# Performance work log

Hardware: AMD Instinct MI355X
Metric: run time of the kernel (lower is better)

Reference implementation:

```python
import jax, jax.numpy as jnp
import numpy as np

N_NODES = 50000
N_EDGES = 800000
D = 128          # input_dim == output_dim
H = 2 * D        # hidden size = 2*output_dim
EPS = 1e-5       # BatchNorm1d eps


def _mlp(x, W1, b1, g1, beta1, W2, b2):
    # Linear -> BatchNorm1d (training-mode batch stats) -> ReLU -> Linear
    y = x @ W1 + b1
    mu = jnp.mean(y, axis=0)
    var = jnp.mean(jnp.square(y - mu), axis=0)  # biased var, as used for normalization
    y = (y - mu) * jax.lax.rsqrt(var + EPS) * g1 + beta1
    y = jax.nn.relu(y)
    return y @ W2 + b2


def setup_inputs() -> dict:
    key = jax.random.key(0)
    ks = jax.random.split(key, 16)
    h = jax.random.normal(ks[0], (N_NODES, D), dtype=jnp.float32)
    e = jax.random.normal(ks[1], (N_EDGES, D), dtype=jnp.float32)
    src = jax.random.randint(ks[2], (N_EDGES,), 0, N_NODES, dtype=jnp.int32)
    dst = jax.random.randint(ks[3], (N_EDGES,), 0, N_NODES, dtype=jnp.int32)

    def lin(k, fan_in, fan_out):
        return jax.random.normal(k, (fan_in, fan_out), dtype=jnp.float32) * (1.0 / np.sqrt(fan_in))

    params = {
        # mlp_bond: in 2D -> H -> D
        'W1b': lin(ks[4], 2 * D, H), 'b1b': jnp.zeros((H,), jnp.float32),
        'g1b': jnp.ones((H,), jnp.float32), 'beta1b': jnp.zeros((H,), jnp.float32),
        'W2b': lin(ks[5], H, D), 'b2b': jnp.zeros((D,), jnp.float32),
        # mlp_atom: in 2D -> H -> D
        'W1a': lin(ks[6], 2 * D, H), 'b1a': jnp.zeros((H,), jnp.float32),
        'g1a': jnp.ones((H,), jnp.float32), 'beta1a': jnp.zeros((H,), jnp.float32),
        'W2a': lin(ks[7], H, D), 'b2a': jnp.zeros((D,), jnp.float32),
    }
    return {'h': h, 'e': e, 'src': src, 'dst': dst, **params}


def reference(h, e, src, dst,
              W1b, b1b, g1b, beta1b, W2b, b2b,
              W1a, b1a, g1a, beta1a, W2a, b2a):
    # --- bond update: gather u_add_v, concat with e, MLP ---
    sum_h_edge = h[src] + h[dst]                              # [E, D]
    e_new = _mlp(jnp.concatenate([sum_h_edge, e], axis=-1),
                 W1b, b1b, g1b, beta1b, W2b, b2b)             # [E, D]

    # --- atom update: scatter-sum of src node feats and NEW edge feats to dst ---
    sum_h = jax.ops.segment_sum(h[src], dst, num_segments=N_NODES)   # copy_u + sum
    sum_e = jax.ops.segment_sum(e_new, dst, num_segments=N_NODES)   # copy_e + sum
    h_new = _mlp(jnp.concatenate([sum_h, sum_e], axis=-1),
                 W1a, b1a, g1a, beta1a, W2a, b2a)             # [N, D]

    # out_batch_norm=False, out_activation=None, residual=False, dropout=None
    return h_new, e_new
```

## Files before the change

kernel.cpp:

```cpp
#include <hip/hip_runtime.h>
#include <hip/hip_bf16.h>
#include <stdint.h>

#define DD 128
#define HH 256
#define EPSBN 1e-5f

typedef __attribute__((ext_vector_type(4))) float f32x4;
typedef __attribute__((ext_vector_type(8))) short s16x8;
typedef __attribute__((ext_vector_type(4))) short s16x4;

__device__ __forceinline__ unsigned short f2bf(float f){
  union { __hip_bfloat16 h; unsigned short u; } v;
  v.h = __float2bfloat16(f);
  return v.u;
}
__device__ __forceinline__ float bf2f(unsigned short s){
  union{unsigned u; float f;} v; v.u=((unsigned)s)<<16; return v.f;
}
__device__ __forceinline__ int swz(int row, int kb){ return row*512 + (kb ^ ((row&31)<<4)); }

__global__ void wt_kernel(const float* __restrict__ W1b, const float* __restrict__ W2b,
                          const float* __restrict__ W1a, const float* __restrict__ W2a,
                          unsigned short* __restrict__ WT1b, unsigned short* __restrict__ WT2b,
                          unsigned short* __restrict__ WT1a, unsigned short* __restrict__ WT2a){
  int idx = blockIdx.x*256 + threadIdx.x;
  if (idx < 65536){ int n=idx>>8, k=idx&255; WT1b[n*256+k]=f2bf(W1b[k*256+n]); }
  else if (idx < 98304){ int t=idx-65536; int n=t>>8, k=t&255; WT2b[n*256+k]=f2bf(W2b[k*128+n]); }
  else if (idx < 163840){ int t=idx-98304; int n=t>>8, k=t&255; WT1a[n*256+k]=f2bf(W1a[k*256+n]); }
  else if (idx < 196608){ int t=idx-163840; int n=t>>8, k=t&255; WT2a[n*256+k]=f2bf(W2a[k*128+n]); }
}

__global__ void h2bf_kernel(const float* __restrict__ h, unsigned short* __restrict__ hb, int n8){
  int i = blockIdx.x*256 + threadIdx.x;
  if (i < n8){
    f32x4 a = *(const f32x4*)(h + (size_t)i*8);
    f32x4 b = *(const f32x4*)(h + (size_t)i*8 + 4);
    s16x8 p;
    #pragma unroll
    for (int q=0;q<4;q++){ p[q]=(short)f2bf(a[q]); p[4+q]=(short)f2bf(b[q]); }
    *(s16x8*)(hb + (size_t)i*8) = p;
  }
}

__global__ void hist_kernel(const int* __restrict__ dst, int* __restrict__ counts, int E){
  int i = blockIdx.x*256 + threadIdx.x;
  if (i < E) atomicAdd(&counts[dst[i]], 1);
}

__global__ void scan_kernel(const int* __restrict__ counts, int* __restrict__ offsets,
                            int* __restrict__ cursor, int n){
  __shared__ int wsum[16];
  int tid = threadIdx.x, lane = tid&63, wid = tid>>6;
  int carry = 0;
  int nch = (n + 1023)/1024;
  for (int ch=0; ch<nch; ch++){
    int i = ch*1024 + tid;
    int v = (i<n)? counts[i] : 0;
    int s = v;
    #pragma unroll
    for (int off=1; off<64; off<<=1){ int t = __shfl_up(s, off); if (lane>=off) s += t; }
    if (lane==63) wsum[wid] = s;
    __syncthreads();
    int woff = 0, tot = 0;
    #pragma unroll
    for (int w=0; w<16; w++){ int t = wsum[w]; if (w<wid) woff += t; tot += t; }
    if (i<n){ int excl = carry + woff + s - v; offsets[i]=excl; cursor[i]=excl; }
    carry += tot;
    __syncthreads();
  }
  if (tid==0) offsets[n] = carry;
}

__global__ void fill_kernel(const int* __restrict__ dst, int* __restrict__ cursor,
                            int* __restrict__ eids, int E){
  int i = blockIdx.x*256 + threadIdx.x;
  if (i < E){ int slot = atomicAdd(&cursor[dst[i]], 1); eids[slot] = i; }
}

__device__ __forceinline__ void gemm1_core(char* xt, const s16x8 (&Bf)[8][2],
                                           float bias0, float bias1,
                                           unsigned short* __restrict__ yout,
                                           float* __restrict__ stats,
                                           int base, int nrows)
{
  const int tid = threadIdx.x;
  const int l = tid&63, w = tid>>6, lr = l&15, lg = l>>4;
  const int nb = w*32;
  f32x4 acc[4][2];
  #pragma unroll
  for (int mt=0;mt<4;mt++)
    #pragma unroll
    for (int nt=0;nt<2;nt++) acc[mt][nt] = (f32x4){0.f,0.f,0.f,0.f};
  #pragma unroll
  for (int kc=0;kc<8;kc++){
    s16x8 af[4];
    #pragma unroll
    for (int mt=0;mt<4;mt++)
      af[mt] = *(const s16x8*)(xt + swz(mt*16 + lr, kc*64 + lg*16));
    #pragma unroll
    for (int nt=0;nt<2;nt++)
      #pragma unroll
      for (int mt=0;mt<4;mt++)
        acc[mt][nt] = __builtin_amdgcn_mfma_f32_16x16x32_bf16(af[mt], Bf[kc][nt], acc[mt][nt], 0,0,0);
  }
  float st1a=0.f, st1b=0.f, st2a=0.f, st2b=0.f;
  #pragma unroll
  for (int mt=0;mt<4;mt++)
    #pragma unroll
    for (int q=0;q<4;q++){
      float m = (base + mt*16 + lg*4 + q < nrows) ? 1.0f : 0.0f;
      float v0 = (acc[mt][0][q] + bias0)*m;
      float v1 = (acc[mt][1][q] + bias1)*m;
      st1a += v0; st2a += v0*v0;
      st1b += v1; st2b += v1*v1;
    }
  __syncthreads();
  #pragma unroll
  for (int mt=0;mt<4;mt++)
    #pragma unroll
    for (int q=0;q<4;q++){
      *(unsigned short*)(xt + (mt*16 + lg*4 + q)*512 + (nb + lr)*2)      = f2bf(acc[mt][0][q] + bias0);
      *(unsigned short*)(xt + (mt*16 + lg*4 + q)*512 + (nb + 16 + lr)*2) = f2bf(acc[mt][1][q] + bias1);
    }
  __syncthreads();
  #pragma unroll
  for (int it=0;it<4;it++){
    int off = it*8192 + tid*16;
    int row = off >> 9;
    if (base + row < nrows)
      *(s16x8*)((char*)yout + (size_t)base*512 + off) = *(const s16x8*)(xt + off);
  }
  {
    int rep = blockIdx.x & 63;
    float s;
    s = st1a; s += __shfl_xor(s,16); s += __shfl_xor(s,32);
    if (l < 16) atomicAdd(&stats[rep*512 + nb + lr], s);
    s = st2a; s += __shfl_xor(s,16); s += __shfl_xor(s,32);
    if (l < 16) atomicAdd(&stats[rep*512 + 256 + nb + lr], s);
    s = st1b; s += __shfl_xor(s,16); s += __shfl_xor(s,32);
    if (l < 16) atomicAdd(&stats[rep*512 + nb + 16 + lr], s);
    s = st2b; s += __shfl_xor(s,16); s += __shfl_xor(s,32);
    if (l < 16) atomicAdd(&stats[rep*512 + 256 + nb + 16 + lr], s);
  }
}

__global__ __launch_bounds__(512, 4) void edge_mlp1(
    const unsigned short* __restrict__ hb, const float* __restrict__ e,
    const int* __restrict__ src, const int* __restrict__ dstv,
    const unsigned short* __restrict__ WT1, const float* __restrict__ b1,
    unsigned short* __restrict__ yout, float* __restrict__ stats, int E)
{
  __shared__ alignas(16) char xt[32768];
  const int tid = threadIdx.x;
  const int l = tid&63, w = tid>>6, lr = l&15, lg = l>>4;
  const int nb = w*32;
  const int base = blockIdx.x*64;

  {
    const int cb = tid&31, r0 = tid>>5;
    #pragma unroll
    for (int k=0;k<4;k++){
      int r = r0 + k*16;
      f32x4 v = *(const f32x4*)(e + (size_t)(base+r)*DD + cb*4);
      s16x4 p;
      #pragma unroll
      for (int q=0;q<4;q++) p[q] = (short)f2bf(v[q]);
      *(s16x4*)(xt + swz(r, 256 + cb*8)) = p;
    }
  }
  {
    const int r = tid>>3, jj = tid&7;
    const int ei = base + r;
    int s_ = src[ei], d_ = dstv[ei];
    const s16x8* hs = (const s16x8*)(hb + (size_t)s_*DD) + jj*2;
    const s16x8* hd = (const s16x8*)(hb + (size_t)d_*DD) + jj*2;
    s16x8 a0=hs[0], a1=hs[1], c0=hd[0], c1=hd[1];
    s16x8 o0, o1;
    #pragma unroll
    for (int q=0;q<8;q++){
      o0[q] = (short)f2bf(bf2f((unsigned short)a0[q]) + bf2f((unsigned short)c0[q]));
      o1[q] = (short)f2bf(bf2f((unsigned short)a1[q]) + bf2f((unsigned short)c1[q]));
    }
    *(s16x8*)(xt + swz(r, jj*32))      = o0;
    *(s16x8*)(xt + swz(r, jj*32 + 16)) = o1;
  }
  s16x8 Bf[8][2];
  #pragma unroll
  for (int kc=0;kc<8;kc++)
    #pragma unroll
    for (int nt=0;nt<2;nt++)
      Bf[kc][nt] = *(const s16x8*)(WT1 + (size_t)(nb + nt*16 + lr)*256 + kc*32 + lg*8);
  float bias0 = b1[nb+lr], bias1 = b1[nb+16+lr];
  __syncthreads();
  gemm1_core(xt, Bf, bias0, bias1, yout, stats, base, E);
}

__global__ __launch_bounds__(512, 2) void node_mlp1(
    const unsigned short* __restrict__ hb, const float* __restrict__ enew,
    const int* __restrict__ src, const int* __restrict__ offsets, const int* __restrict__ eids,
    const unsigned short* __restrict__ WT1, const float* __restrict__ b1,
    unsigned short* __restrict__ yout, float* __restrict__ stats, int NN)
{
  __shared__ alignas(16) char xt[32768];
  const int tid = threadIdx.x;
  const int l = tid&63, w = tid>>6, lr = l&15, lg = l>>4;
  const int nb = w*32;
  const int base = blockIdx.x*64;
  const int r = tid>>3, jj = tid&7;
  const int node = base + r;

  float ah[16], ae[16];
  #pragma unroll
  for (int q=0;q<16;q++){ ah[q]=0.f; ae[q]=0.f; }
  if (node < NN){
    int beg = offsets[node], end = offsets[node+1];
    for (int p=beg;p<end;p++){
      int eid = eids[p];
      int s_ = src[eid];
      const s16x8* hs = (const s16x8*)(hb + (size_t)s_*DD + jj*16);
      const f32x4* ep = (const f32x4*)(enew + (size_t)eid*DD + jj*16);
      s16x8 a0 = hs[0], a1 = hs[1];
      f32x4 e0 = ep[0], e1 = ep[1], e2 = ep[2], e3 = ep[3];
      #pragma unroll
      for (int q=0;q<8;q++){ ah[q] += bf2f((unsigned short)a0[q]); ah[8+q] += bf2f((unsigned short)a1[q]); }
      #pragma unroll
      for (int q=0;q<4;q++){ ae[q] += e0[q]; ae[4+q] += e1[q]; ae[8+q] += e2[q]; ae[12+q] += e3[q]; }
    }
  }
  {
    s16x8 o0, o1;
    #pragma unroll
    for (int q=0;q<8;q++){ o0[q] = (short)f2bf(ah[q]); o1[q] = (short)f2bf(ah[8+q]); }
    *(s16x8*)(xt + swz(r, jj*32))      = o0;
    *(s16x8*)(xt + swz(r, jj*32 + 16)) = o1;
    #pragma unroll
    for (int q=0;q<8;q++){ o0[q] = (short)f2bf(ae[q]); o1[q] = (short)f2bf(ae[8+q]); }
    *(s16x8*)(xt + swz(r, 256 + jj*32))      = o0;
    *(s16x8*)(xt + swz(r, 256 + jj*32 + 16)) = o1;
  }
  s16x8 Bf[8][2];
  #pragma unroll
  for (int kc=0;kc<8;kc++)
    #pragma unroll
    for (int nt=0;nt<2;nt++)
      Bf[kc][nt] = *(const s16x8*)(WT1 + (size_t)(nb + nt*16 + lr)*256 + kc*32 + lg*8);
  float bias0 = b1[nb+lr], bias1 = b1[nb+16+lr];
  __syncthreads();
  gemm1_core(xt, Bf, bias0, bias1, yout, stats, base, NN);
}

__global__ void finalize_kernel(const float* __restrict__ stats, const float* __restrict__ g,
                                const float* __restrict__ beta, float* __restrict__ scale, float invcnt){
  __shared__ float red[512];
  int tid = threadIdx.x;
  float s = 0.f;
  for (int rep=0; rep<64; rep++) s += stats[rep*512 + tid];
  red[tid] = s;
  __syncthreads();
  if (tid < 256){
    float mu  = red[tid]*invcnt;
    float var = red[256+tid]*invcnt - mu*mu;
    float a = g[tid] * rsqrtf(var + EPSBN);
    float c = beta[tid] - mu*a;
    scale[2*tid] = a; scale[2*tid+1] = c;
  }
}

__global__ __launch_bounds__(512, 4) void mlp2_kernel(const unsigned short* y,
    const unsigned short* __restrict__ WT2, const float* __restrict__ b2,
    const float* __restrict__ scale, float* outp, int nrows)
{
  __shared__ alignas(16) char xt[32768];
  const int tid = threadIdx.x;
  const int l = tid&63, w = tid>>6, lr = l&15, lg = l>>4;
  const int nb = w*16;
  const int base0 = blockIdx.x*128;

  s16x8 Bf[8];
  #pragma unroll
  for (int kc=0;kc<8;kc++)
    Bf[kc] = *(const s16x8*)(WT2 + (size_t)(nb + lr)*HH + kc*32 + lg*8);
  float bias = b2[nb+lr];
  const int cb = tid&31, r0 = tid>>5;
  float sa[8], sc[8];
  #pragma unroll
  for (int q=0;q<8;q++){ sa[q]=scale[2*(cb*8+q)]; sc[q]=scale[2*(cb*8+q)+1]; }

  #pragma unroll 1
  for (int t=0;t<2;t++){
    const int base = base0 + t*64;
    #pragma unroll
    for (int k=0;k<4;k++){
      int r = r0 + k*16;
      s16x8 raw = {0,0,0,0,0,0,0,0};
      if (base + r < nrows) raw = *(const s16x8*)(y + (size_t)(base+r)*HH + cb*8);
      s16x8 o;
      #pragma unroll
      for (int q=0;q<8;q++){
        float f = fmaxf(bf2f((unsigned short)raw[q])*sa[q] + sc[q], 0.0f);
        o[q] = (short)f2bf(f);
      }
      *(s16x8*)(xt + swz(r, cb*16)) = o;
    }
    __syncthreads();
    f32x4 acc[4];
    #pragma unroll
    for (int mt=0;mt<4;mt++) acc[mt] = (f32x4){0.f,0.f,0.f,0.f};
    #pragma unroll
    for (int kc=0;kc<8;kc++){
      s16x8 af[4];
      #pragma unroll
      for (int mt=0;mt<4;mt++)
        af[mt] = *(const s16x8*)(xt + swz(mt*16 + lr, kc*64 + lg*16));
      #pragma unroll
      for (int mt=0;mt<4;mt++)
        acc[mt] = __builtin_amdgcn_mfma_f32_16x16x32_bf16(af[mt], Bf[kc], acc[mt], 0,0,0);
    }
    __syncthreads();
    #pragma unroll
    for (int mt=0;mt<4;mt++)
      #pragma unroll
      for (int q=0;q<4;q++)
        *(float*)(xt + (mt*16 + lg*4 + q)*512 + (nb + lr)*4) = acc[mt][q] + bias;
    __syncthreads();
    #pragma unroll
    for (int it=0;it<4;it++){
      int off = it*8192 + tid*16;
      int row = off >> 9;
      if (base + row < nrows)
        *(f32x4*)(outp + (size_t)(base+row)*DD + ((off&511)>>2)) = *(const f32x4*)(xt + off);
    }
    if (t==0) __syncthreads();
  }
}

extern "C" void kernel_launch(void* const* d_in, const int* in_sizes, int n_in,
                              void* d_out, int out_size, void* d_ws, size_t ws_size,
                              hipStream_t stream) {
  const float* h    = (const float*)d_in[0];
  const float* e    = (const float*)d_in[1];
  const int*   src  = (const int*)d_in[2];
  const int*   dst  = (const int*)d_in[3];
  const float* W1b  = (const float*)d_in[4];
  const float* b1b  = (const float*)d_in[5];
  const float* g1b  = (const float*)d_in[6];
  const float* beta1b=(const float*)d_in[7];
  const float* W2b  = (const float*)d_in[8];
  const float* b2b  = (const float*)d_in[9];
  const float* W1a  = (const float*)d_in[10];
  const float* b1a  = (const float*)d_in[11];
  const float* g1a  = (const float*)d_in[12];
  const float* beta1a=(const float*)d_in[13];
  const float* W2a  = (const float*)d_in[14];
  const float* b2a  = (const float*)d_in[15];

  const int E  = in_sizes[2];
  const int NN = in_sizes[0] / DD;

  char* ws = (char*)d_ws;
  unsigned short* WT1b = (unsigned short*)(ws + 0);
  unsigned short* WT2b = (unsigned short*)(ws + 131072);
  unsigned short* WT1a = (unsigned short*)(ws + 196608);
  unsigned short* WT2a = (unsigned short*)(ws + 327680);
  float* scaleE = (float*)(ws + 393216);
  float* scaleN = (float*)(ws + 395264);
  float* statsE = (float*)(ws + 397312);
  float* statsN = (float*)(ws + 528384);
  int* counts  = (int*)(ws + 659456);
  int* offsets = (int*)(ws + 860160);
  int* cursor  = (int*)(ws + 1060864);
  int* eids    = (int*)(ws + 1261568);
  unsigned short* ya = (unsigned short*)(ws + 4461568);
  unsigned short* hb = (unsigned short*)(ws + 30086144);

  float* outH = (float*)d_out;
  float* outE = outH + (size_t)NN * DD;
  unsigned short* yE = (unsigned short*)outE;

  hipMemsetAsync(ws + 397312, 0, 131072 + 131072 + 200704, stream);

  wt_kernel<<<768, 256, 0, stream>>>(W1b, W2b, W1a, W2a, WT1b, WT2b, WT1a, WT2a);
  h2bf_kernel<<<(NN*DD/8 + 255)/256, 256, 0, stream>>>(h, hb, NN*DD/8);
  hist_kernel<<<(E+255)/256, 256, 0, stream>>>(dst, counts, E);
  scan_kernel<<<1, 1024, 0, stream>>>(counts, offsets, cursor, NN);
  fill_kernel<<<(E+255)/256, 256, 0, stream>>>(dst, cursor, eids, E);

  const int tE64  = E/64;
  const int tE128 = E/128;
  const int tN64  = (NN + 63)/64;
  const int tN128 = (NN + 127)/128;

  edge_mlp1<<<tE64, 512, 0, stream>>>(hb, e, src, dst, WT1b, b1b, yE, statsE, E);
  finalize_kernel<<<1, 512, 0, stream>>>(statsE, g1b, beta1b, scaleE, 1.0f/(float)E);
  mlp2_kernel<<<tE128, 512, 0, stream>>>(yE, WT2b, b2b, scaleE, outE, E);
  node_mlp1<<<tN64, 512, 0, stream>>>(hb, outE, src, offsets, eids, WT1a, b1a, ya, statsN, NN);
  finalize_kernel<<<1, 512, 0, stream>>>(statsN, g1a, beta1a, scaleN, 1.0f/(float)NN);
  mlp2_kernel<<<tN128, 512, 0, stream>>>(ya, WT2a, b2a, scaleN, outH, NN);
}
```

Baseline: 799.0 us.

## Split node gather from node GEMM, pre-sort src ids, fuse histogram

```diff
diff --git a/kernel.cpp b/kernel.cpp
--- a/kernel.cpp
+++ b/kernel.cpp
@@ -31,7 +31,8 @@
   else if (idx < 196608){ int t=idx-163840; int n=t>>8, k=t&255; WT2a[n*256+k]=f2bf(W2a[k*128+n]); }
 }
 
-__global__ void h2bf_kernel(const float* __restrict__ h, unsigned short* __restrict__ hb, int n8){
+__global__ void h2bf_hist_kernel(const float* __restrict__ h, unsigned short* __restrict__ hb, int n8,
+                                 const int* __restrict__ dst, int* __restrict__ counts, int E){
   int i = blockIdx.x*256 + threadIdx.x;
   if (i < n8){
     f32x4 a = *(const f32x4*)(h + (size_t)i*8);
@@ -41,10 +42,6 @@
     for (int q=0;q<4;q++){ p[q]=(short)f2bf(a[q]); p[4+q]=(short)f2bf(b[q]); }
     *(s16x8*)(hb + (size_t)i*8) = p;
   }
-}
-
-__global__ void hist_kernel(const int* __restrict__ dst, int* __restrict__ counts, int E){
-  int i = blockIdx.x*256 + threadIdx.x;
   if (i < E) atomicAdd(&counts[dst[i]], 1);
 }
 
@@ -72,10 +69,15 @@
   if (tid==0) offsets[n] = carry;
 }
 
-__global__ void fill_kernel(const int* __restrict__ dst, int* __restrict__ cursor,
-                            int* __restrict__ eids, int E){
+__global__ void fill_kernel(const int* __restrict__ dst, const int* __restrict__ srcv,
+                            int* __restrict__ cursor,
+                            int* __restrict__ eids, int* __restrict__ esrc, int E){
   int i = blockIdx.x*256 + threadIdx.x;
-  if (i < E){ int slot = atomicAdd(&cursor[dst[i]], 1); eids[slot] = i; }
+  if (i < E){
+    int slot = atomicAdd(&cursor[dst[i]], 1);
+    eids[slot] = i;
+    esrc[slot] = srcv[i];
+  }
 }
 
 __device__ __forceinline__ void gemm1_core(char* xt, const s16x8 (&Bf)[8][2],
@@ -196,9 +198,50 @@
   gemm1_core(xt, Bf, bias0, bias1, yout, stats, base, E);
 }
 
-__global__ __launch_bounds__(512, 2) void node_mlp1(
+__global__ __launch_bounds__(256, 8) void node_gather(
     const unsigned short* __restrict__ hb, const float* __restrict__ enew,
-    const int* __restrict__ src, const int* __restrict__ offsets, const int* __restrict__ eids,
+    const int* __restrict__ offsets, const int* __restrict__ eids, const int* __restrict__ esrc,
+    unsigned short* __restrict__ xnode, int NN)
+{
+  const int tid = threadIdx.x;
+  const int r = tid>>3, jj = tid&7;
+  const int node = blockIdx.x*32 + r;
+  if (node >= NN) return;
+  float ah[16], ae[16];
+  #pragma unroll
+  for (int q=0;q<16;q++){ ah[q]=0.f; ae[q]=0.f; }
+  int beg = offsets[node], end = offsets[node+1];
+  if (beg < end){
+    int eid = eids[beg];
+    int s_  = esrc[beg];
+    for (int p = beg; p < end; p++){
+      int pn = (p+1 < end) ? p+1 : p;
+      int eid_n = eids[pn];
+      int s_n   = esrc[pn];
+      const s16x8* hs = (const s16x8*)(hb + (size_t)s_*DD + jj*16);
+      const f32x4* ep = (const f32x4*)(enew + (size_t)eid*DD + jj*16);
+      s16x8 a0 = hs[0], a1 = hs[1];
+      f32x4 e0 = ep[0], e1 = ep[1], e2 = ep[2], e3 = ep[3];
+      #pragma unroll
+      for (int q=0;q<8;q++){ ah[q] += bf2f((unsigned short)a0[q]); ah[8+q] += bf2f((unsigned short)a1[q]); }
+      #pragma unroll
+      for (int q=0;q<4;q++){ ae[q] += e0[q]; ae[4+q] += e1[q]; ae[8+q] += e2[q]; ae[12+q] += e3[q]; }
+      eid = eid_n; s_ = s_n;
+    }
+  }
+  s16x8 o0, o1;
+  #pragma unroll
+  for (int q=0;q<8;q++){ o0[q] = (short)f2bf(ah[q]); o1[q] = (short)f2bf(ah[8+q]); }
+  *(s16x8*)(xnode + (size_t)node*HH + jj*16)     = o0;
+  *(s16x8*)(xnode + (size_t)node*HH + jj*16 + 8) = o1;
+  #pragma unroll
+  for (int q=0;q<8;q++){ o0[q] = (short)f2bf(ae[q]); o1[q] = (short)f2bf(ae[8+q]); }
+  *(s16x8*)(xnode + (size_t)node*HH + 128 + jj*16)     = o0;
+  *(s16x8*)(xnode + (size_t)node*HH + 128 + jj*16 + 8) = o1;
+}
+
+__global__ __launch_bounds__(512, 4) void node_gemm1(
+    const unsigned short* __restrict__ xnode,
     const unsigned short* __restrict__ WT1, const float* __restrict__ b1,
     unsigned short* __restrict__ yout, float* __restrict__ stats, int NN)
 {
@@ -207,37 +250,14 @@
   const int l = tid&63, w = tid>>6, lr = l&15, lg = l>>4;
   const int nb = w*32;
   const int base = blockIdx.x*64;
-  const int r = tid>>3, jj = tid&7;
-  const int node = base + r;
-
-  float ah[16], ae[16];
-  #pragma unroll
-  for (int q=0;q<16;q++){ ah[q]=0.f; ae[q]=0.f; }
-  if (node < NN){
-    int beg = offsets[node], end = offsets[node+1];
-    for (int p=beg;p<end;p++){
-      int eid = eids[p];
-      int s_ = src[eid];
-      const s16x8* hs = (const s16x8*)(hb + (size_t)s_*DD + jj*16);
-      const f32x4* ep = (const f32x4*)(enew + (size_t)eid*DD + jj*16);
-      s16x8 a0 = hs[0], a1 = hs[1];
-      f32x4 e0 = ep[0], e1 = ep[1], e2 = ep[2], e3 = ep[3];
-      #pragma unroll
-      for (int q=0;q<8;q++){ ah[q] += bf2f((unsigned short)a0[q]); ah[8+q] += bf2f((unsigned short)a1[q]); }
-      #pragma unroll
-      for (int q=0;q<4;q++){ ae[q] += e0[q]; ae[4+q] += e1[q]; ae[8+q] += e2[q]; ae[12+q] += e3[q]; }
-    }
-  }
-  {
-    s16x8 o0, o1;
-    #pragma unroll
-    for (int q=0;q<8;q++){ o0[q] = (short)f2bf(ah[q]); o1[q] = (short)f2bf(ah[8+q]); }
-    *(s16x8*)(xt + swz(r, jj*32))      = o0;
-    *(s16x8*)(xt + swz(r, jj*32 + 16)) = o1;
-    #pragma unroll
-    for (int q=0;q<8;q++){ o0[q] = (short)f2bf(ae[q]); o1[q] = (short)f2bf(ae[8+q]); }
-    *(s16x8*)(xt + swz(r, 256 + jj*32))      = o0;
-    *(s16x8*)(xt + swz(r, 256 + jj*32 + 16)) = o1;
+
+  #pragma unroll
+  for (int it=0;it<4;it++){
+    int off = it*8192 + tid*16;
+    int row = off >> 9, kb = off & 511;
+    s16x8 v = {0,0,0,0,0,0,0,0};
+    if (base + row < NN) v = *(const s16x8*)((const char*)xnode + (size_t)base*512 + off);
+    *(s16x8*)(xt + swz(row, kb)) = v;
   }
   s16x8 Bf[8][2];
   #pragma unroll
@@ -373,28 +393,31 @@
   int* eids    = (int*)(ws + 1261568);
   unsigned short* ya = (unsigned short*)(ws + 4461568);
   unsigned short* hb = (unsigned short*)(ws + 30086144);
+  int* esrc   = (int*)(ws + 42886144);
 
   float* outH = (float*)d_out;
   float* outE = outH + (size_t)NN * DD;
   unsigned short* yE = (unsigned short*)outE;
+  unsigned short* xnode = (unsigned short*)outH;
 
   hipMemsetAsync(ws + 397312, 0, 131072 + 131072 + 200704, stream);
 
   wt_kernel<<<768, 256, 0, stream>>>(W1b, W2b, W1a, W2a, WT1b, WT2b, WT1a, WT2a);
-  h2bf_kernel<<<(NN*DD/8 + 255)/256, 256, 0, stream>>>(h, hb, NN*DD/8);
-  hist_kernel<<<(E+255)/256, 256, 0, stream>>>(dst, counts, E);
+  h2bf_hist_kernel<<<(NN*DD/8 + 255)/256, 256, 0, stream>>>(h, hb, NN*DD/8, dst, counts, E);
   scan_kernel<<<1, 1024, 0, stream>>>(counts, offsets, cursor, NN);
-  fill_kernel<<<(E+255)/256, 256, 0, stream>>>(dst, cursor, eids, E);
+  fill_kernel<<<(E+255)/256, 256, 0, stream>>>(dst, src, cursor, eids, esrc, E);
 
   const int tE64  = E/64;
   const int tE128 = E/128;
   const int tN64  = (NN + 63)/64;
   const int tN128 = (NN + 127)/128;
+  const int gG    = (NN + 31)/32;
 
   edge_mlp1<<<tE64, 512, 0, stream>>>(hb, e, src, dst, WT1b, b1b, yE, statsE, E);
   finalize_kernel<<<1, 512, 0, stream>>>(statsE, g1b, beta1b, scaleE, 1.0f/(float)E);
   mlp2_kernel<<<tE128, 512, 0, stream>>>(yE, WT2b, b2b, scaleE, outE, E);
-  node_mlp1<<<tN64, 512, 0, stream>>>(hb, outE, src, offsets, eids, WT1a, b1a, ya, statsN, NN);
+  node_gather<<<gG, 256, 0, stream>>>(hb, outE, offsets, eids, esrc, xnode, NN);
+  node_gemm1<<<tN64, 512, 0, stream>>>(xnode, WT1a, b1a, ya, statsN, NN);
   finalize_kernel<<<1, 512, 0, stream>>>(statsN, g1a, beta1a, scaleN, 1.0f/(float)NN);
   mlp2_kernel<<<tN128, 512, 0, stream>>>(ya, WT2a, b2a, scaleN, outH, NN);
 }
```

Result: slower. 841.6 us (+5.3%).
